# Kernel tuning notes

Hardware: AMD Instinct MI355X
Metric: run time of the kernel (lower is better)

## Reference

```python
import jax, jax.numpy as jnp
import numpy as np

BS, L, DIM = 16, 2048, 512
NUM_GROUPS, NUM_CODES = 2, 320
CODE_DIM = 256
VAR_DIM = CODE_DIM // NUM_GROUPS  # 128
INNER = DIM * 2                    # projFactor=2
TAU = 2.0                          # max(maxTemp*decay**0, minTemp) at numUpdates=0


def setup_inputs() -> dict:
    key = jax.random.key(0)
    ks = jax.random.split(key, 7)
    x = jax.random.normal(ks[0], (BS, L, DIM), jnp.float32)
    # gumbels = -log(Exp(1)) == standard Gumbel noise, matching torch's exponential_().log().neg()
    gumbels = jax.random.gumbel(ks[1], (BS * L * NUM_GROUPS, NUM_CODES), jnp.float32)
    W1 = jax.random.normal(ks[2], (DIM, INNER), jnp.float32) * (1.0 / np.sqrt(DIM))
    b1 = jnp.zeros((INNER,), jnp.float32)
    W2 = jax.random.normal(ks[3], (INNER, NUM_GROUPS * NUM_CODES), jnp.float32) * (1.0 / np.sqrt(INNER))
    b2 = jnp.zeros((NUM_GROUPS * NUM_CODES,), jnp.float32)
    # nn.init.uniform_ on embeddings: U[0,1); combineGroups=True -> single shared codebook (numCodes, varDim)
    emb = jax.random.uniform(ks[4], (NUM_CODES, VAR_DIM), jnp.float32)
    return {"x": x, "gumbels": gumbels, "W1": W1, "b1": b1, "W2": W2, "b2": b2, "emb": emb}


def reference(x, gumbels, W1, b1, W2, b2, emb):
    bs, l, d = x.shape
    xt = x.reshape(bs * l, d)
    h = jax.nn.gelu(xt @ W1 + b1, approximate=False)          # (N, INNER), torch GELU is exact erf
    logits = (h @ W2 + b2).reshape(bs * l * NUM_GROUPS, NUM_CODES)
    # training path: gumbel-softmax with straight-through hard one-hot
    soft = jax.nn.softmax((logits + gumbels) / TAU, axis=-1)  # (N*G, C)
    idx = jnp.argmax(soft, axis=-1)
    hard = jax.nn.one_hot(idx, NUM_CODES, dtype=soft.dtype)
    st = hard + soft - jax.lax.stop_gradient(soft)            # straight-through estimator
    st = st.reshape(bs * l, NUM_GROUPS, NUM_CODES)
    # combineGroups=True: embeddings repeated per group == shared codebook; the
    # (broadcast-mul).sum(-2) in torch is exactly this contraction (no huge intermediate).
    out = jnp.einsum('ngc,cd->ngd', st, emb)                  # (N, G, varDim)
    return out.reshape(bs, l, NUM_GROUPS * VAR_DIM)
```

## Files before the change

kernel.cpp:

```cpp
#include <hip/hip_runtime.h>
#include <math.h>


#define NTOK   32768
#define DIM    512
#define INNER  1024
#define NC     320
#define NGRP   2
#define VD     128
#define OUTD   256
#define RCAP   2048
#define W1F_OFF (1u<<20)
#define W2F_OFF (1u<<21)
#define HD_OFF  (1u<<22)
#define MARGIN 8.0e-3f
#define SMEM_BYTES (65536 + 3328)

typedef _Float16 half8 __attribute__((ext_vector_type(8)));
typedef _Float16 half4 __attribute__((ext_vector_type(4)));
typedef float    f32x4 __attribute__((ext_vector_type(4)));

#define W1F_N (16 * 64 * 64)
#define W2F_N (32 * 40 * 64)
__global__ void prep_kernel(const float* __restrict__ W1, const float* __restrict__ W2,
                            _Float16* __restrict__ W1F, _Float16* __restrict__ W2F,
                            unsigned* __restrict__ cnt) {
  const int o = blockIdx.x * 256 + threadIdx.x;
  if (o == 0) cnt[0] = 0u;
  if (o < W1F_N) {
    const int l = o & 63, ib = (o >> 6) & 63, ks = o >> 12;
    const int inner = ib * 16 + (l & 15);
    const int kb = ks * 32 + (l >> 4) * 8;
    _Float16* d = W1F + (size_t)o * 8;
#pragma unroll
    for (int j = 0; j < 8; ++j)
      d[j] = (_Float16)W1[(size_t)(kb + j) * INNER + inner];
  } else {
    const int o2 = o - W1F_N;
    if (o2 < W2F_N) {
      const int l = o2 & 63, cb = (o2 >> 6) % 40, ks = o2 / (40 * 64);
      const int code = cb * 16 + (l & 15);
      const int kb = ks * 32 + (l >> 4) * 8;
      _Float16* d = W2F + (size_t)o2 * 8;
#pragma unroll
      for (int j = 0; j < 8; ++j)
        d[j] = (_Float16)W2[(size_t)(kb + j) * (NC * NGRP) + code];
    }
  }
}

__device__ __forceinline__ float gelu_f(float s) {
  return 0.5f * s * (1.0f + erff(s * 0.70710678118654752440f));
}

__global__ __launch_bounds__(512, 4)
void fused_kernel(const float* __restrict__ x, const float* __restrict__ gum,
                  const _Float16* __restrict__ W1F, const _Float16* __restrict__ W2F,
                  const float* __restrict__ b1, const float* __restrict__ b2,
                  const float* __restrict__ emb, float* __restrict__ out,
                  unsigned* __restrict__ cnt, unsigned* __restrict__ list) {
  extern __shared__ char smem[];
  float*    redm1 = (float*)(smem + 65536);
  float*    redm2 = (float*)(smem + 65536 + 1024);
  unsigned* redi  = (unsigned*)(smem + 65536 + 2048);
  unsigned* idxs  = (unsigned*)(smem + 65536 + 3072);

  const int tid = threadIdx.x;
  const int w   = tid >> 6;
  const int l   = tid & 63;
  const int l15 = l & 15;
  const int lq  = l >> 4;
  const int T0  = blockIdx.x << 5;

#pragma unroll
  for (int i = 0; i < 8; ++i) {
    const int q = tid + i * 512;
    const int row = q >> 7;
    const int c = (q & 127) << 2;
    const float4 v = *(const float4*)(x + (size_t)(T0 + row) * DIM + c);
    half4 hv; hv[0] = (_Float16)v.x; hv[1] = (_Float16)v.y;
    hv[2] = (_Float16)v.z; hv[3] = (_Float16)v.w;
    const unsigned byte = ((unsigned)(row * 1024 + c * 2)) ^ ((unsigned)(row & 7) << 4);
    *(half4*)(smem + byte) = hv;
  }
  __syncthreads();

  {
    f32x4 acc[8][2];
#pragma unroll
    for (int i = 0; i < 8; ++i)
#pragma unroll
      for (int j = 0; j < 2; ++j) { f32x4 z = {0.f,0.f,0.f,0.f}; acc[i][j] = z; }

    const _Float16* w1f = W1F + (size_t)(w * 8) * 512 + (size_t)l * 8;
    for (int ks = 0; ks < 16; ++ks) {
      const int k0 = ks * 32;
      half8 a[8], bf[2];
#pragma unroll
      for (int mt = 0; mt < 8; ++mt)
        a[mt] = *(const half8*)(w1f + (size_t)(ks * 64 + mt) * 512);
#pragma unroll
      for (int nt = 0; nt < 2; ++nt) {
        const int token = nt * 16 + l15;
        const unsigned byte = ((unsigned)(token * 1024 + (k0 + lq * 8) * 2))
                              ^ ((unsigned)(token & 7) << 4);
        bf[nt] = *(const half8*)(smem + byte);
      }
#pragma unroll
      for (int mt = 0; mt < 8; ++mt)
#pragma unroll
        for (int nt = 0; nt < 2; ++nt)
          acc[mt][nt] = __builtin_amdgcn_mfma_f32_16x16x32_f16(a[mt], bf[nt], acc[mt][nt], 0, 0, 0);
    }
    __syncthreads();

#pragma unroll
    for (int mt = 0; mt < 8; ++mt) {
      const int inner0 = w * 128 + mt * 16 + lq * 4;
      const float4 bv = *(const float4*)(b1 + inner0);
#pragma unroll
      for (int nt = 0; nt < 2; ++nt) {
        const int token = nt * 16 + l15;
        const f32x4 v = acc[mt][nt];
        half4 hv;
        hv[0] = (_Float16)gelu_f(v[0] + bv.x);
        hv[1] = (_Float16)gelu_f(v[1] + bv.y);
        hv[2] = (_Float16)gelu_f(v[2] + bv.z);
        hv[3] = (_Float16)gelu_f(v[3] + bv.w);
        const unsigned byte = ((unsigned)(token * 2048 + inner0 * 2))
                              ^ ((unsigned)(token & 7) << 4);
        *(half4*)(smem + byte) = hv;
      }
    }
  }
  __syncthreads();

  const int g = w >> 2;
  {
    f32x4 acc[5][2];
#pragma unroll
    for (int i = 0; i < 5; ++i)
#pragma unroll
      for (int j = 0; j < 2; ++j) { f32x4 z = {0.f,0.f,0.f,0.f}; acc[i][j] = z; }

    const _Float16* w2f = W2F + (size_t)(w * 5) * 512 + (size_t)l * 8;
    for (int ks = 0; ks < 32; ++ks) {
      const int k0 = ks * 32;
      half8 a[5], bf[2];
#pragma unroll
      for (int mt = 0; mt < 5; ++mt)
        a[mt] = *(const half8*)(w2f + (size_t)(ks * 40 + mt) * 512);
#pragma unroll
      for (int nt = 0; nt < 2; ++nt) {
        const int token = nt * 16 + l15;
        const unsigned byte = ((unsigned)(token * 2048 + (k0 + lq * 8) * 2))
                              ^ ((unsigned)(token & 7) << 4);
        bf[nt] = *(const half8*)(smem + byte);
      }
#pragma unroll
      for (int mt = 0; mt < 5; ++mt)
#pragma unroll
        for (int nt = 0; nt < 2; ++nt)
          acc[mt][nt] = __builtin_amdgcn_mfma_f32_16x16x32_f16(a[mt], bf[nt], acc[mt][nt], 0, 0, 0);
    }

    float m1v[2] = {-1e30f,-1e30f};
    float m2v[2] = {-1e30f,-1e30f};
    unsigned i1v[2] = {0,0};
#pragma unroll
    for (int mt = 0; mt < 5; ++mt) {
      const int code0 = w * 80 + mt * 16 + lq * 4;
      const int cg0 = code0 - g * NC;
      const float4 b2v = *(const float4*)(b2 + code0);
#pragma unroll
      for (int nt = 0; nt < 2; ++nt) {
        const int tokg = T0 + nt * 16 + l15;
        const float4 gv = *(const float4*)(gum + ((size_t)tokg * 2 + g) * NC + cg0);
        const f32x4 v = acc[mt][nt];
        const float ss[4] = {v[0] + b2v.x + gv.x, v[1] + b2v.y + gv.y,
                             v[2] + b2v.z + gv.z, v[3] + b2v.w + gv.w};
#pragma unroll
        for (int r = 0; r < 4; ++r) {
          const float sv = ss[r];
          const unsigned cc = (unsigned)(cg0 + r);
          if (sv > m1v[nt]) { m2v[nt] = m1v[nt]; m1v[nt] = sv; i1v[nt] = cc; }
          else if (sv > m2v[nt]) m2v[nt] = sv;
        }
      }
    }
#pragma unroll
    for (int mask = 16; mask <= 32; mask <<= 1) {
#pragma unroll
      for (int nt = 0; nt < 2; ++nt) {
        const float om1 = __shfl_xor(m1v[nt], mask);
        const float om2 = __shfl_xor(m2v[nt], mask);
        const unsigned oi = (unsigned)__shfl_xor((int)i1v[nt], mask);
        const bool take = (om1 > m1v[nt]) || (om1 == m1v[nt] && oi < i1v[nt]);
        if (take) { m2v[nt] = fmaxf(m1v[nt], om2); m1v[nt] = om1; i1v[nt] = oi; }
        else      { m2v[nt] = fmaxf(m2v[nt], om1); }
      }
    }
    if (l < 16) {
#pragma unroll
      for (int nt = 0; nt < 2; ++nt) {
        const int tok = nt * 16 + l15;
        redm1[w * 32 + tok] = m1v[nt];
        redm2[w * 32 + tok] = m2v[nt];
        redi [w * 32 + tok] = i1v[nt];
      }
    }
  }
  __syncthreads();

  if (tid < 64) {
    const int pg = tid >> 5;
    const int tok = tid & 31;
    float m1 = -1e30f, m2 = -1e30f; unsigned i1 = 0;
#pragma unroll
    for (int k = 0; k < 4; ++k) {
      const int ww = pg * 4 + k;
      const float a1 = redm1[ww * 32 + tok];
      const float a2 = redm2[ww * 32 + tok];
      const unsigned ai = redi[ww * 32 + tok];
      if (a1 > m1) { m2 = fmaxf(m1, a2); m1 = a1; i1 = ai; }
      else         { m2 = fmaxf(m2, a1); }
    }
    idxs[tid] = i1;
    if (m1 - m2 < MARGIN) {
      const unsigned pos = atomicAdd(cnt, 1u);
      if (pos < RCAP) list[pos] = (unsigned)(((T0 + tok) << 1) | pg);
    }
  }
  __syncthreads();

#pragma unroll
  for (int i = 0; i < 4; ++i) {
    const int q = tid + i * 512;
    const int p = q >> 5;
    const int dd = q & 31;
    const int pg = p >> 5;
    const int tok = p & 31;
    const unsigned idx = idxs[p];
    *(float4*)(out + (size_t)(T0 + tok) * OUTD + pg * VD + dd * 4)
      = *(const float4*)(emb + (size_t)idx * VD + dd * 4);
  }
}

__global__ __launch_bounds__(512, 4)
void refine1_kernel(const float* __restrict__ x, const float* __restrict__ W1,
                    const float* __restrict__ b1,
                    const unsigned* __restrict__ cnt, const unsigned* __restrict__ list,
                    float* __restrict__ hdws) {
  __shared__ float xs[DIM];
  unsigned n = cnt[0]; if (n > RCAP) n = RCAP;
  const unsigned e = blockIdx.x;
  if (e >= n) return;
  const unsigned tok = list[e] >> 1;
  const int tid = threadIdx.x;
  xs[tid] = x[(size_t)tok * DIM + tid];
  __syncthreads();

  double a0 = 0.0, a1 = 0.0, c0 = 0.0, c1 = 0.0;
#pragma unroll 4
  for (int k = 0; k < DIM; k += 2) {
    const double x0 = (double)xs[k], x1 = (double)xs[k + 1];
    const float* r0 = W1 + (size_t)k * INNER + tid;
    const float* r1 = W1 + (size_t)(k + 1) * INNER + tid;
    a0 += x0 * (double)r0[0];
    a1 += x0 * (double)r0[512];
    c0 += x1 * (double)r1[0];
    c1 += x1 * (double)r1[512];
  }
  const double s0 = a0 + c0 + (double)b1[tid];
  const double s1 = a1 + c1 + (double)b1[tid + 512];
  hdws[(size_t)e * INNER + tid]       = (float)(0.5 * s0 * (1.0 + erf(s0 * 0.70710678118654752440)));
  hdws[(size_t)e * INNER + tid + 512] = (float)(0.5 * s1 * (1.0 + erf(s1 * 0.70710678118654752440)));
}

__global__ __launch_bounds__(320, 4)
void refine2_kernel(const float* __restrict__ gum, const float* __restrict__ W2,
                    const float* __restrict__ b2, const float* __restrict__ emb,
                    float* __restrict__ out,
                    const unsigned* __restrict__ cnt, const unsigned* __restrict__ list,
                    const float* __restrict__ hdws) {
  __shared__ float hs[INNER];
  __shared__ double wv[5];
  __shared__ int wi[5];
  __shared__ int best;
  unsigned n = cnt[0]; if (n > RCAP) n = RCAP;
  const unsigned e = blockIdx.x;
  if (e >= n) return;
  const unsigned tok = list[e] >> 1;
  const int g = (int)(list[e] & 1u);
  const int tid = threadIdx.x;

  for (int j = tid; j < INNER; j += 320) hs[j] = hdws[(size_t)e * INNER + j];
  __syncthreads();

  const float* w2c = W2 + (size_t)g * NC + tid;
  double acc = 0.0, accb = 0.0;
#pragma unroll 4
  for (int k = 0; k < INNER; k += 2) {
    acc  += (double)hs[k]     * (double)w2c[(size_t)k * (NC * NGRP)];
    accb += (double)hs[k + 1] * (double)w2c[(size_t)(k + 1) * (NC * NGRP)];
  }
  double v = acc + accb + (double)b2[g * NC + tid]
                        + (double)gum[((size_t)tok * 2 + g) * NC + tid];
  int bi = tid;
#pragma unroll
  for (int m = 1; m < 64; m <<= 1) {
    const double ov = __shfl_xor(v, m);
    const int oi = __shfl_xor(bi, m);
    if (ov > v || (ov == v && oi < bi)) { v = ov; bi = oi; }
  }
  if ((tid & 63) == 0) { wv[tid >> 6] = v; wi[tid >> 6] = bi; }
  __syncthreads();
  if (tid == 0) {
    double bv = wv[0]; int bb = wi[0];
#pragma unroll
    for (int k = 1; k < 5; ++k)
      if (wv[k] > bv || (wv[k] == bv && wi[k] < bb)) { bv = wv[k]; bb = wi[k]; }
    best = bb;
  }
  __syncthreads();
  if (tid < VD)
    out[(size_t)tok * OUTD + g * VD + tid] = emb[(size_t)best * VD + tid];
}

__global__ __launch_bounds__(512, 1)
void refine_kernel(const float* __restrict__ x, const float* __restrict__ gum,
                   const float* __restrict__ W1, const float* __restrict__ b1,
                   const float* __restrict__ W2, const float* __restrict__ b2,
                   const float* __restrict__ emb, float* __restrict__ out,
                   const unsigned* __restrict__ cnt, const unsigned* __restrict__ list) {
  __shared__ double xs[4][DIM];
  __shared__ double hd[4][INNER];
  __shared__ double sc[4][NC];
  __shared__ int amax[4];
  const int tid = threadIdx.x;
  unsigned n = cnt[0];
  if (n > RCAP) n = RCAP;

  for (unsigned base = blockIdx.x * 4u; base < n; base += gridDim.x * 4u) {
    const int nb = (int)((n - base) < 4u ? (n - base) : 4u);
    unsigned ng[4];
#pragma unroll
    for (int e = 0; e < 4; ++e) ng[e] = list[base + (e < nb ? e : 0)];

    for (int e = 0; e < nb; ++e)
      xs[e][tid] = (double)x[(size_t)(ng[e] >> 1) * DIM + tid];
    __syncthreads();

#pragma unroll
    for (int jj = 0; jj < 2; ++jj) {
      const int j = tid + jj * 512;
      double a0 = 0, a1 = 0, a2 = 0, a3 = 0;
      for (int k = 0; k < DIM; ++k) {
        const double wvv = (double)W1[(size_t)k * INNER + j];
        a0 += xs[0][k] * wvv; a1 += xs[1][k] * wvv;
        a2 += xs[2][k] * wvv; a3 += xs[3][k] * wvv;
      }
      const double bb = (double)b1[j];
      const double s0 = a0 + bb, s1 = a1 + bb, s2 = a2 + bb, s3 = a3 + bb;
      hd[0][j] = 0.5 * s0 * (1.0 + erf(s0 * 0.70710678118654752440));
      hd[1][j] = 0.5 * s1 * (1.0 + erf(s1 * 0.70710678118654752440));
      hd[2][j] = 0.5 * s2 * (1.0 + erf(s2 * 0.70710678118654752440));
      hd[3][j] = 0.5 * s3 * (1.0 + erf(s3 * 0.70710678118654752440));
    }
    __syncthreads();

    for (int task = tid; task < 4 * NC; task += 512) {
      const int e = task / NC;
      const int c = task - e * NC;
      if (e < nb) {
        const unsigned tok = ng[e] >> 1;
        const int gg = (int)(ng[e] & 1u);
        const float* w2c = W2 + (size_t)gg * NC + c;
        double acc = 0.0;
        for (int k = 0; k < INNER; ++k)
          acc += hd[e][k] * (double)w2c[(size_t)k * (NC * NGRP)];
        sc[e][c] = acc + (double)b2[gg * NC + c]
                       + (double)gum[((size_t)tok * 2 + gg) * NC + c];
      }
    }
    __syncthreads();

    if (tid < 4 && tid < nb) {
      double bestv = sc[tid][0]; int bi = 0;
      for (int c = 1; c < NC; ++c)
        if (sc[tid][c] > bestv) { bestv = sc[tid][c]; bi = c; }
      amax[tid] = bi;
    }
    __syncthreads();

    {
      const int e = tid >> 7;
      const int d = tid & 127;
      if (e < nb) {
        const unsigned tok = ng[e] >> 1;
        const int gg = (int)(ng[e] & 1u);
        out[(size_t)tok * OUTD + gg * VD + d] = emb[(size_t)amax[e] * VD + d];
      }
    }
    __syncthreads();
  }
}

extern "C" void kernel_launch(void* const* d_in, const int* in_sizes, int n_in,
                              void* d_out, int out_size, void* d_ws, size_t ws_size,
                              hipStream_t stream) {
  (void)in_sizes; (void)n_in; (void)out_size;
  const float* x   = (const float*)d_in[0];
  const float* gum = (const float*)d_in[1];
  const float* W1  = (const float*)d_in[2];
  const float* b1  = (const float*)d_in[3];
  const float* W2  = (const float*)d_in[4];
  const float* b2  = (const float*)d_in[5];
  const float* emb = (const float*)d_in[6];
  float* out = (float*)d_out;
  char* ws = (char*)d_ws;
  unsigned* cnt  = (unsigned*)ws;
  unsigned* list = (unsigned*)(ws + 16);
  _Float16* W1F = (_Float16*)(ws + W1F_OFF);
  _Float16* W2F = (_Float16*)(ws + W2F_OFF);
  float* hdws = (float*)(ws + HD_OFF);

  hipFuncSetAttribute((const void*)fused_kernel,
                      hipFuncAttributeMaxDynamicSharedMemorySize, SMEM_BYTES);

  const int prep_items = W1F_N + W2F_N;
  prep_kernel<<<(prep_items + 255) / 256, 256, 0, stream>>>(W1, W2, W1F, W2F, cnt);
  fused_kernel<<<NTOK / 32, 512, SMEM_BYTES, stream>>>(x, gum, W1F, W2F, b1, b2,
                                                       emb, out, cnt, list);
  const bool big_ws = ws_size >= (size_t)HD_OFF + (size_t)RCAP * INNER * sizeof(float);
  if (big_ws) {
    refine1_kernel<<<RCAP, 512, 0, stream>>>(x, W1, b1, cnt, list, hdws);
    refine2_kernel<<<RCAP, 320, 0, stream>>>(gum, W2, b2, emb, out, cnt, list, hdws);
  } else {
    refine_kernel<<<256, 512, 0, stream>>>(x, gum, W1, b1, W2, b2, emb, out, cnt, list);
  }
}
```

Before: 269.2 us.

## Split fused MLP into tiled fp16 GEMM kernels with LDS-direct loads

Replaces the per-32-token fused kernel with separate kernels: a prep pass converting x and weights to fp16, a 128x128-tiled GEMM1 with GELU writing h to workspace, a tiled GEMM2 computing per-tile top-2 partials, and a reduce kernel that picks the argmax and gathers embeddings. Loads go through global_load_lds into swizzled shared memory. The aim is more weight reuse per block and better MFMA utilisation. The cost is extra global round trips for xh, h and the partials, plus more kernel launches. The old fused path is kept as a fallback for small workspaces.

```diff
diff --git a/kernel.cpp b/kernel.cpp
--- a/kernel.cpp
+++ b/kernel.cpp
@@ -10,239 +10,294 @@
 #define VD     128
 #define OUTD   256
 #define RCAP   2048
+#define MARGIN 8.0e-3f
+
+#define L_LIST 16u
+#define L_W1T  (64u<<10)
+#define L_W2T  (2u<<20)
+#define L_XH   (4u<<20)
+#define L_H    (36u<<20)
+#define L_PART (100u<<20)
+#define L_HDW  (104u<<20)
+#define WS_NEED (120u<<20)
+
 #define W1F_OFF (1u<<20)
 #define W2F_OFF (1u<<21)
-#define HD_OFF  (1u<<22)
-#define MARGIN 8.0e-3f
 #define SMEM_BYTES (65536 + 3328)
 
 typedef _Float16 half8 __attribute__((ext_vector_type(8)));
 typedef _Float16 half4 __attribute__((ext_vector_type(4)));
 typedef float    f32x4 __attribute__((ext_vector_type(4)));
 
-#define W1F_N (16 * 64 * 64)
-#define W2F_N (32 * 40 * 64)
-__global__ void prep_kernel(const float* __restrict__ W1, const float* __restrict__ W2,
-                            _Float16* __restrict__ W1F, _Float16* __restrict__ W2F,
-                            unsigned* __restrict__ cnt) {
+__device__ __forceinline__ float gelu_f(float s) {
+  return 0.5f * s * (1.0f + erff(s * 0.70710678118654752440f));
+}
+
+#if defined(__has_builtin) && __has_builtin(__builtin_amdgcn_global_load_lds)
+#define GLOAD16(gp, ldsbase, lane) \
+  __builtin_amdgcn_global_load_lds((const __attribute__((address_space(1))) void*)(gp), \
+                                   (__attribute__((address_space(3))) void*)(ldsbase), 16, 0, 0)
+#else
+#define GLOAD16(gp, ldsbase, lane) \
+  do { *(uint4*)((char*)(ldsbase) + (lane) * 16) = *(const uint4*)(gp); } while (0)
+#endif
+
+#define XH_JOBS   2097152
+#define W1T_JOBS  65536
+#define W2T_JOBS  81920
+#define PREP_JOBS (XH_JOBS + W1T_JOBS + W2T_JOBS)
+__global__ __launch_bounds__(256)
+void prep2_kernel(const float* __restrict__ x, const float* __restrict__ W1,
+                  const float* __restrict__ W2, _Float16* __restrict__ xh,
+                  _Float16* __restrict__ W1T, _Float16* __restrict__ W2T,
+                  unsigned* __restrict__ cnt) {
   const int o = blockIdx.x * 256 + threadIdx.x;
   if (o == 0) cnt[0] = 0u;
-  if (o < W1F_N) {
-    const int l = o & 63, ib = (o >> 6) & 63, ks = o >> 12;
-    const int inner = ib * 16 + (l & 15);
-    const int kb = ks * 32 + (l >> 4) * 8;
-    _Float16* d = W1F + (size_t)o * 8;
+  if (o < XH_JOBS) {
+    const float4 v0 = *(const float4*)(x + (size_t)o * 8);
+    const float4 v1 = *(const float4*)(x + (size_t)o * 8 + 4);
+    half8 hv;
+    hv[0] = (_Float16)v0.x; hv[1] = (_Float16)v0.y; hv[2] = (_Float16)v0.z; hv[3] = (_Float16)v0.w;
+    hv[4] = (_Float16)v1.x; hv[5] = (_Float16)v1.y; hv[6] = (_Float16)v1.z; hv[7] = (_Float16)v1.w;
+    *(half8*)(xh + (size_t)o * 8) = hv;
+  } else if (o < XH_JOBS + W1T_JOBS) {
+    const int q = o - XH_JOBS;
+    const int i = q >> 6, k0 = (q & 63) * 8;
 #pragma unroll
     for (int j = 0; j < 8; ++j)
-      d[j] = (_Float16)W1[(size_t)(kb + j) * INNER + inner];
-  } else {
-    const int o2 = o - W1F_N;
-    if (o2 < W2F_N) {
-      const int l = o2 & 63, cb = (o2 >> 6) % 40, ks = o2 / (40 * 64);
-      const int code = cb * 16 + (l & 15);
-      const int kb = ks * 32 + (l >> 4) * 8;
-      _Float16* d = W2F + (size_t)o2 * 8;
-#pragma unroll
-      for (int j = 0; j < 8; ++j)
-        d[j] = (_Float16)W2[(size_t)(kb + j) * (NC * NGRP) + code];
-    }
-  }
-}
-
-__device__ __forceinline__ float gelu_f(float s) {
-  return 0.5f * s * (1.0f + erff(s * 0.70710678118654752440f));
-}
-
-__global__ __launch_bounds__(512, 4)
-void fused_kernel(const float* __restrict__ x, const float* __restrict__ gum,
-                  const _Float16* __restrict__ W1F, const _Float16* __restrict__ W2F,
-                  const float* __restrict__ b1, const float* __restrict__ b2,
-                  const float* __restrict__ emb, float* __restrict__ out,
-                  unsigned* __restrict__ cnt, unsigned* __restrict__ list) {
-  extern __shared__ char smem[];
-  float*    redm1 = (float*)(smem + 65536);
-  float*    redm2 = (float*)(smem + 65536 + 1024);
-  unsigned* redi  = (unsigned*)(smem + 65536 + 2048);
-  unsigned* idxs  = (unsigned*)(smem + 65536 + 3072);
-
+      W1T[(size_t)i * DIM + k0 + j] = (_Float16)W1[(size_t)(k0 + j) * INNER + i];
+  } else if (o < PREP_JOBS) {
+    const int q = o - XH_JOBS - W1T_JOBS;
+    const int c = q >> 7, i0 = (q & 127) * 8;
+#pragma unroll
+    for (int j = 0; j < 8; ++j)
+      W2T[(size_t)c * INNER + i0 + j] = (_Float16)W2[(size_t)(i0 + j) * (NC * NGRP) + c];
+  }
+}
+
+__global__ __launch_bounds__(256, 4)
+void gemm1_kernel(const _Float16* __restrict__ xh, const _Float16* __restrict__ W1T,
+                  const float* __restrict__ b1, _Float16* __restrict__ h) {
+  __shared__ char smem[32768];
   const int tid = threadIdx.x;
-  const int w   = tid >> 6;
-  const int l   = tid & 63;
-  const int l15 = l & 15;
-  const int lq  = l >> 4;
-  const int T0  = blockIdx.x << 5;
-
-#pragma unroll
-  for (int i = 0; i < 8; ++i) {
-    const int q = tid + i * 512;
-    const int row = q >> 7;
-    const int c = (q & 127) << 2;
-    const float4 v = *(const float4*)(x + (size_t)(T0 + row) * DIM + c);
-    half4 hv; hv[0] = (_Float16)v.x; hv[1] = (_Float16)v.y;
-    hv[2] = (_Float16)v.z; hv[3] = (_Float16)v.w;
-    const unsigned byte = ((unsigned)(row * 1024 + c * 2)) ^ ((unsigned)(row & 7) << 4);
-    *(half4*)(smem + byte) = hv;
-  }
-  __syncthreads();
-
-  {
-    f32x4 acc[8][2];
-#pragma unroll
-    for (int i = 0; i < 8; ++i)
-#pragma unroll
-      for (int j = 0; j < 2; ++j) { f32x4 z = {0.f,0.f,0.f,0.f}; acc[i][j] = z; }
-
-    const _Float16* w1f = W1F + (size_t)(w * 8) * 512 + (size_t)l * 8;
-    for (int ks = 0; ks < 16; ++ks) {
-      const int k0 = ks * 32;
-      half8 a[8], bf[2];
-#pragma unroll
-      for (int mt = 0; mt < 8; ++mt)
-        a[mt] = *(const half8*)(w1f + (size_t)(ks * 64 + mt) * 512);
-#pragma unroll
-      for (int nt = 0; nt < 2; ++nt) {
-        const int token = nt * 16 + l15;
-        const unsigned byte = ((unsigned)(token * 1024 + (k0 + lq * 8) * 2))
-                              ^ ((unsigned)(token & 7) << 4);
-        bf[nt] = *(const half8*)(smem + byte);
-      }
-#pragma unroll
-      for (int mt = 0; mt < 8; ++mt)
-#pragma unroll
-        for (int nt = 0; nt < 2; ++nt)
-          acc[mt][nt] = __builtin_amdgcn_mfma_f32_16x16x32_f16(a[mt], bf[nt], acc[mt][nt], 0, 0, 0);
-    }
-    __syncthreads();
-
-#pragma unroll
-    for (int mt = 0; mt < 8; ++mt) {
-      const int inner0 = w * 128 + mt * 16 + lq * 4;
-      const float4 bv = *(const float4*)(b1 + inner0);
-#pragma unroll
-      for (int nt = 0; nt < 2; ++nt) {
-        const int token = nt * 16 + l15;
-        const f32x4 v = acc[mt][nt];
-        half4 hv;
-        hv[0] = (_Float16)gelu_f(v[0] + bv.x);
-        hv[1] = (_Float16)gelu_f(v[1] + bv.y);
-        hv[2] = (_Float16)gelu_f(v[2] + bv.z);
-        hv[3] = (_Float16)gelu_f(v[3] + bv.w);
-        const unsigned byte = ((unsigned)(token * 2048 + inner0 * 2))
-                              ^ ((unsigned)(token & 7) << 4);
-        *(half4*)(smem + byte) = hv;
-      }
-    }
-  }
-  __syncthreads();
-
-  const int g = w >> 2;
-  {
-    f32x4 acc[5][2];
-#pragma unroll
-    for (int i = 0; i < 5; ++i)
-#pragma unroll
-      for (int j = 0; j < 2; ++j) { f32x4 z = {0.f,0.f,0.f,0.f}; acc[i][j] = z; }
-
-    const _Float16* w2f = W2F + (size_t)(w * 5) * 512 + (size_t)l * 8;
-    for (int ks = 0; ks < 32; ++ks) {
-      const int k0 = ks * 32;
-      half8 a[5], bf[2];
-#pragma unroll
-      for (int mt = 0; mt < 5; ++mt)
-        a[mt] = *(const half8*)(w2f + (size_t)(ks * 40 + mt) * 512);
-#pragma unroll
-      for (int nt = 0; nt < 2; ++nt) {
-        const int token = nt * 16 + l15;
-        const unsigned byte = ((unsigned)(token * 2048 + (k0 + lq * 8) * 2))
-                              ^ ((unsigned)(token & 7) << 4);
-        bf[nt] = *(const half8*)(smem + byte);
-      }
-#pragma unroll
-      for (int mt = 0; mt < 5; ++mt)
-#pragma unroll
-        for (int nt = 0; nt < 2; ++nt)
-          acc[mt][nt] = __builtin_amdgcn_mfma_f32_16x16x32_f16(a[mt], bf[nt], acc[mt][nt], 0, 0, 0);
-    }
-
-    float m1v[2] = {-1e30f,-1e30f};
-    float m2v[2] = {-1e30f,-1e30f};
-    unsigned i1v[2] = {0,0};
-#pragma unroll
-    for (int mt = 0; mt < 5; ++mt) {
-      const int code0 = w * 80 + mt * 16 + lq * 4;
-      const int cg0 = code0 - g * NC;
-      const float4 b2v = *(const float4*)(b2 + code0);
-#pragma unroll
-      for (int nt = 0; nt < 2; ++nt) {
-        const int tokg = T0 + nt * 16 + l15;
-        const float4 gv = *(const float4*)(gum + ((size_t)tokg * 2 + g) * NC + cg0);
-        const f32x4 v = acc[mt][nt];
-        const float ss[4] = {v[0] + b2v.x + gv.x, v[1] + b2v.y + gv.y,
-                             v[2] + b2v.z + gv.z, v[3] + b2v.w + gv.w};
-#pragma unroll
-        for (int r = 0; r < 4; ++r) {
-          const float sv = ss[r];
-          const unsigned cc = (unsigned)(cg0 + r);
-          if (sv > m1v[nt]) { m2v[nt] = m1v[nt]; m1v[nt] = sv; i1v[nt] = cc; }
-          else if (sv > m2v[nt]) m2v[nt] = sv;
+  const int w = tid >> 6, l = tid & 63;
+  const int l15 = l & 15, lq = l >> 4;
+  const int bid = blockIdx.x;
+  const int bn = bid & 7, bm = bid >> 3;
+  const int wm = w >> 1, wn = w & 1;
+
+  const int r0 = (w * 2 + 0) * 16 + (l >> 2);
+  const int r1 = (w * 2 + 1) * 16 + (l >> 2);
+  const int c0 = (((l & 3) ^ (r0 & 3)) * 8);
+  const int c1 = (((l & 3) ^ (r1 & 3)) * 8);
+  const _Float16* gA0 = xh  + (size_t)(bm * 128 + r0) * DIM + c0;
+  const _Float16* gA1 = xh  + (size_t)(bm * 128 + r1) * DIM + c1;
+  const _Float16* gB0 = W1T + (size_t)(bn * 128 + r0) * DIM + c0;
+  const _Float16* gB1 = W1T + (size_t)(bn * 128 + r1) * DIM + c1;
+  char* lA0 = smem + (w * 2 + 0) * 1024;
+  char* lA1 = smem + (w * 2 + 1) * 1024;
+  char* lB0 = smem + 8192 + (w * 2 + 0) * 1024;
+  char* lB1 = smem + 8192 + (w * 2 + 1) * 1024;
+
+  f32x4 acc[4][4];
+#pragma unroll
+  for (int i = 0; i < 4; ++i)
+#pragma unroll
+    for (int j = 0; j < 4; ++j) { f32x4 z = {0.f, 0.f, 0.f, 0.f}; acc[i][j] = z; }
+
+  const int swz = (lq ^ (l15 & 3)) << 4;
+  const int aoff = (wm * 64 + l15) * 64 + swz;
+  const int boff = 8192 + (wn * 64 + l15) * 64 + swz;
+
+  for (int ks = 0; ks < 16; ++ks) {
+    __syncthreads();
+    GLOAD16(gA0 + ks * 32, lA0, l);
+    GLOAD16(gA1 + ks * 32, lA1, l);
+    GLOAD16(gB0 + ks * 32, lB0, l);
+    GLOAD16(gB1 + ks * 32, lB1, l);
+    __syncthreads();
+    half8 a[4], b[4];
+#pragma unroll
+    for (int mi = 0; mi < 4; ++mi) a[mi] = *(const half8*)(smem + aoff + mi * 1024);
+#pragma unroll
+    for (int ni = 0; ni < 4; ++ni) b[ni] = *(const half8*)(smem + boff + ni * 1024);
+#pragma unroll
+    for (int mi = 0; mi < 4; ++mi)
+#pragma unroll
+      for (int ni = 0; ni < 4; ++ni)
+        acc[mi][ni] = __builtin_amdgcn_mfma_f32_16x16x32_f16(a[mi], b[ni], acc[mi][ni], 0, 0, 0);
+  }
+  __syncthreads();
+
+  _Float16* eT = (_Float16*)smem;
+  float bb[4];
+#pragma unroll
+  for (int ni = 0; ni < 4; ++ni) bb[ni] = b1[bn * 128 + wn * 64 + ni * 16 + l15];
+#pragma unroll
+  for (int mi = 0; mi < 4; ++mi) {
+    const int row = wm * 64 + mi * 16 + lq * 4;
+#pragma unroll
+    for (int ni = 0; ni < 4; ++ni) {
+      const int col = wn * 64 + ni * 16 + l15;
+#pragma unroll
+      for (int r = 0; r < 4; ++r)
+        eT[(row + r) * 128 + col] = (_Float16)gelu_f(acc[mi][ni][r] + bb[ni]);
+    }
+  }
+  __syncthreads();
+#pragma unroll
+  for (int it = 0; it < 8; ++it) {
+    const int s = tid + it * 256;
+    const int row = s >> 4, i8 = s & 15;
+    *(half8*)(h + (size_t)(bm * 128 + row) * INNER + bn * 128 + i8 * 8)
+        = *(const half8*)(eT + row * 128 + i8 * 8);
+  }
+}
+
+__global__ __launch_bounds__(256, 4)
+void gemm2_kernel(const _Float16* __restrict__ h, const _Float16* __restrict__ W2T,
+                  const float* __restrict__ b2, const float* __restrict__ gum,
+                  unsigned* __restrict__ part) {
+  __shared__ char smem[32768];
+  const int tid = threadIdx.x;
+  const int w = tid >> 6, l = tid & 63;
+  const int l15 = l & 15, lq = l >> 4;
+  const int bid = blockIdx.x;
+  const int bt = bid % 5, bm = bid / 5;
+  const int wm = w >> 1, wn = w & 1;
+
+  const int r0 = (w * 2 + 0) * 16 + (l >> 2);
+  const int r1 = (w * 2 + 1) * 16 + (l >> 2);
+  const int c0 = (((l & 3) ^ (r0 & 3)) * 8);
+  const int c1 = (((l & 3) ^ (r1 & 3)) * 8);
+  const _Float16* gA0 = h   + (size_t)(bm * 128 + r0) * INNER + c0;
+  const _Float16* gA1 = h   + (size_t)(bm * 128 + r1) * INNER + c1;
+  const _Float16* gB0 = W2T + (size_t)(bt * 128 + r0) * INNER + c0;
+  const _Float16* gB1 = W2T + (size_t)(bt * 128 + r1) * INNER + c1;
+  char* lA0 = smem + (w * 2 + 0) * 1024;
+  char* lA1 = smem + (w * 2 + 1) * 1024;
+  char* lB0 = smem + 8192 + (w * 2 + 0) * 1024;
+  char* lB1 = smem + 8192 + (w * 2 + 1) * 1024;
+
+  f32x4 acc[4][4];
+#pragma unroll
+  for (int i = 0; i < 4; ++i)
+#pragma unroll
+    for (int j = 0; j < 4; ++j) { f32x4 z = {0.f, 0.f, 0.f, 0.f}; acc[i][j] = z; }
+
+  const int swz = (lq ^ (l15 & 3)) << 4;
+  const int aoff = (wm * 64 + l15) * 64 + swz;
+  const int boff = 8192 + (wn * 64 + l15) * 64 + swz;
+
+  for (int ks = 0; ks < 32; ++ks) {
+    __syncthreads();
+    GLOAD16(gA0 + ks * 32, lA0, l);
+    GLOAD16(gA1 + ks * 32, lA1, l);
+    GLOAD16(gB0 + ks * 32, lB0, l);
+    GLOAD16(gB1 + ks * 32, lB1, l);
+    __syncthreads();
+    half8 a[4], b[4];
+#pragma unroll
+    for (int mi = 0; mi < 4; ++mi) a[mi] = *(const half8*)(smem + aoff + mi * 1024);
+#pragma unroll
+    for (int ni = 0; ni < 4; ++ni) b[ni] = *(const half8*)(smem + boff + ni * 1024);
+#pragma unroll
+    for (int mi = 0; mi < 4; ++mi)
+#pragma unroll
+      for (int ni = 0; ni < 4; ++ni)
+        acc[mi][ni] = __builtin_amdgcn_mfma_f32_16x16x32_f16(a[mi], b[ni], acc[mi][ni], 0, 0, 0);
+  }
+
+  float* eF = (float*)smem;
+  const int nm = (bt == 2) ? 8 : 16;
+#pragma unroll
+  for (int half = 0; half < 2; ++half) {
+    __syncthreads();
+    if (wm == half) {
+#pragma unroll
+      for (int mi = 0; mi < 4; ++mi) {
+        const int rl = mi * 16 + lq * 4;
+#pragma unroll
+        for (int ni = 0; ni < 4; ++ni) {
+          const int col = wn * 64 + ni * 16 + l15;
+#pragma unroll
+          for (int r = 0; r < 4; ++r) eF[(rl + r) * 128 + col] = acc[mi][ni][r];
         }
       }
     }
-#pragma unroll
-    for (int mask = 16; mask <= 32; mask <<= 1) {
-#pragma unroll
-      for (int nt = 0; nt < 2; ++nt) {
-        const float om1 = __shfl_xor(m1v[nt], mask);
-        const float om2 = __shfl_xor(m2v[nt], mask);
-        const unsigned oi = (unsigned)__shfl_xor((int)i1v[nt], mask);
-        const bool take = (om1 > m1v[nt]) || (om1 == m1v[nt] && oi < i1v[nt]);
-        if (take) { m2v[nt] = fmaxf(m1v[nt], om2); m1v[nt] = om1; i1v[nt] = oi; }
-        else      { m2v[nt] = fmaxf(m2v[nt], om1); }
-      }
-    }
-    if (l < 16) {
-#pragma unroll
-      for (int nt = 0; nt < 2; ++nt) {
-        const int tok = nt * 16 + l15;
-        redm1[w * 32 + tok] = m1v[nt];
-        redm2[w * 32 + tok] = m2v[nt];
-        redi [w * 32 + tok] = i1v[nt];
-      }
-    }
-  }
-  __syncthreads();
-
-  if (tid < 64) {
-    const int pg = tid >> 5;
-    const int tok = tid & 31;
-    float m1 = -1e30f, m2 = -1e30f; unsigned i1 = 0;
-#pragma unroll
-    for (int k = 0; k < 4; ++k) {
-      const int ww = pg * 4 + k;
-      const float a1 = redm1[ww * 32 + tok];
-      const float a2 = redm2[ww * 32 + tok];
-      const unsigned ai = redi[ww * 32 + tok];
-      if (a1 > m1) { m2 = fmaxf(m1, a2); m1 = a1; i1 = ai; }
-      else         { m2 = fmaxf(m2, a1); }
-    }
-    idxs[tid] = i1;
-    if (m1 - m2 < MARGIN) {
-      const unsigned pos = atomicAdd(cnt, 1u);
-      if (pos < RCAP) list[pos] = (unsigned)(((T0 + tok) << 1) | pg);
-    }
-  }
-  __syncthreads();
-
-#pragma unroll
-  for (int i = 0; i < 4; ++i) {
-    const int q = tid + i * 512;
-    const int p = q >> 5;
-    const int dd = q & 31;
-    const int pg = p >> 5;
-    const int tok = p & 31;
-    const unsigned idx = idxs[p];
-    *(float4*)(out + (size_t)(T0 + tok) * OUTD + pg * VD + dd * 4)
-      = *(const float4*)(emb + (size_t)idx * VD + dd * 4);
+    __syncthreads();
+#pragma unroll
+    for (int it = 0; it < 8; ++it) {
+      const int s = tid + it * 256;
+      const int rl = s >> 5, cc = (s & 31) * 4;
+      const int t = bm * 128 + half * 64 + rl;
+      const float4 lv  = *(const float4*)(eF + rl * 128 + cc);
+      const float4 b2v = *(const float4*)(b2 + bt * 128 + cc);
+      const float4 gv  = *(const float4*)(gum + (size_t)t * 640 + bt * 128 + cc);
+      float m1 = -1e30f, m2 = -1e30f; unsigned i1 = 0;
+      const float vv[4] = {(lv.x + b2v.x) + gv.x, (lv.y + b2v.y) + gv.y,
+                           (lv.z + b2v.z) + gv.z, (lv.w + b2v.w) + gv.w};
+#pragma unroll
+      for (int r = 0; r < 4; ++r) {
+        const unsigned c = (unsigned)(bt * 128 + cc + r);
+        if (vv[r] > m1) { m2 = m1; m1 = vv[r]; i1 = c; }
+        else if (vv[r] > m2) m2 = vv[r];
+      }
+      for (int m = 1; m <= nm; m <<= 1) {
+        const float om1 = __shfl_xor(m1, m);
+        const float om2 = __shfl_xor(m2, m);
+        const unsigned oi = (unsigned)__shfl_xor((int)i1, m);
+        const bool take = (om1 > m1) || (om1 == m1 && oi < i1);
+        if (take) { m2 = fmaxf(m1, om2); m1 = om1; i1 = oi; }
+        else      { m2 = fmaxf(m2, om1); }
+      }
+      const int lr = tid & 31;
+      const bool writer = (bt == 2) ? (lr == 0 || lr == 16) : (lr == 0);
+      if (writer) {
+        int slot;
+        if (bt == 0) slot = 0; else if (bt == 1) slot = 1;
+        else if (bt == 3) slot = 4; else if (bt == 4) slot = 5;
+        else slot = (i1 < (unsigned)NC) ? 2 : 3;
+        const unsigned ing = (i1 < (unsigned)NC) ? i1 : (i1 - NC);
+        unsigned* p = part + ((size_t)t * 6 + slot) * 4;
+        p[0] = __float_as_uint(m1);
+        p[1] = __float_as_uint(m2);
+        p[2] = ing;
+      }
+    }
+  }
+}
+
+__global__ __launch_bounds__(256, 4)
+void reduce_kernel(const unsigned* __restrict__ part, const float* __restrict__ emb,
+                   float* __restrict__ out, unsigned* __restrict__ cnt,
+                   unsigned* __restrict__ list) {
+  __shared__ unsigned idxs[256];
+  const int tid = threadIdx.x;
+  const int pair = blockIdx.x * 256 + tid;
+  const int t = pair >> 1, g = pair & 1;
+  float m1 = -1e30f, m2 = -1e30f; unsigned i1 = 0;
+#pragma unroll
+  for (int s = 0; s < 3; ++s) {
+    const unsigned* p = part + ((size_t)t * 6 + g * 3 + s) * 4;
+    const float a1 = __uint_as_float(p[0]);
+    const float a2 = __uint_as_float(p[1]);
+    const unsigned ai = p[2];
+    if (a1 > m1) { m2 = fmaxf(m1, a2); m1 = a1; i1 = ai; }
+    else         { m2 = fmaxf(m2, a1); }
+  }
+  idxs[tid] = i1;
+  if (m1 - m2 < MARGIN) {
+    const unsigned pos = atomicAdd(cnt, 1u);
+    if (pos < RCAP) list[pos] = (unsigned)((t << 1) | g);
+  }
+  __syncthreads();
+#pragma unroll
+  for (int it = 0; it < 32; ++it) {
+    const int s2 = tid + it * 256;
+    const int p = s2 >> 5, dd = (s2 & 31) * 4;
+    *(float4*)(out + (size_t)blockIdx.x * 32768 + p * 128 + dd)
+        = *(const float4*)(emb + (size_t)idxs[p] * VD + dd);
   }
 }
 
@@ -259,17 +314,16 @@
   const int tid = threadIdx.x;
   xs[tid] = x[(size_t)tok * DIM + tid];
   __syncthreads();
-
   double a0 = 0.0, a1 = 0.0, c0 = 0.0, c1 = 0.0;
 #pragma unroll 4
   for (int k = 0; k < DIM; k += 2) {
     const double x0 = (double)xs[k], x1 = (double)xs[k + 1];
-    const float* r0 = W1 + (size_t)k * INNER + tid;
-    const float* r1 = W1 + (size_t)(k + 1) * INNER + tid;
-    a0 += x0 * (double)r0[0];
-    a1 += x0 * (double)r0[512];
-    c0 += x1 * (double)r1[0];
-    c1 += x1 * (double)r1[512];
+    const float* rr0 = W1 + (size_t)k * INNER + tid;
+    const float* rr1 = W1 + (size_t)(k + 1) * INNER + tid;
+    a0 += x0 * (double)rr0[0];
+    a1 += x0 * (double)rr0[512];
+    c0 += x1 * (double)rr1[0];
+    c1 += x1 * (double)rr1[512];
   }
   const double s0 = a0 + c0 + (double)b1[tid];
   const double s1 = a1 + c1 + (double)b1[tid + 512];
@@ -293,10 +347,8 @@
   const unsigned tok = list[e] >> 1;
   const int g = (int)(list[e] & 1u);
   const int tid = threadIdx.x;
-
   for (int j = tid; j < INNER; j += 320) hs[j] = hdws[(size_t)e * INNER + j];
   __syncthreads();
-
   const float* w2c = W2 + (size_t)g * NC + tid;
   double acc = 0.0, accb = 0.0;
 #pragma unroll 4
@@ -325,6 +377,212 @@
   __syncthreads();
   if (tid < VD)
     out[(size_t)tok * OUTD + g * VD + tid] = emb[(size_t)best * VD + tid];
+}
+
+#define W1F_N (16 * 64 * 64)
+#define W2F_N (32 * 40 * 64)
+__global__ void prep_kernel(const float* __restrict__ W1, const float* __restrict__ W2,
+                            _Float16* __restrict__ W1F, _Float16* __restrict__ W2F,
+                            unsigned* __restrict__ cnt) {
+  const int o = blockIdx.x * 256 + threadIdx.x;
+  if (o == 0) cnt[0] = 0u;
+  if (o < W1F_N) {
+    const int l = o & 63, ib = (o >> 6) & 63, ks = o >> 12;
+    const int inner = ib * 16 + (l & 15);
+    const int kb = ks * 32 + (l >> 4) * 8;
+    _Float16* d = W1F + (size_t)o * 8;
+#pragma unroll
+    for (int j = 0; j < 8; ++j) d[j] = (_Float16)W1[(size_t)(kb + j) * INNER + inner];
+  } else {
+    const int o2 = o - W1F_N;
+    if (o2 < W2F_N) {
+      const int l = o2 & 63, cb = (o2 >> 6) % 40, ks = o2 / (40 * 64);
+      const int code = cb * 16 + (l & 15);
+      const int kb = ks * 32 + (l >> 4) * 8;
+      _Float16* d = W2F + (size_t)o2 * 8;
+#pragma unroll
+      for (int j = 0; j < 8; ++j) d[j] = (_Float16)W2[(size_t)(kb + j) * (NC * NGRP) + code];
+    }
+  }
+}
+
+__global__ __launch_bounds__(512, 4)
+void fused_kernel(const float* __restrict__ x, const float* __restrict__ gum,
+                  const _Float16* __restrict__ W1F, const _Float16* __restrict__ W2F,
+                  const float* __restrict__ b1, const float* __restrict__ b2,
+                  const float* __restrict__ emb, float* __restrict__ out,
+                  unsigned* __restrict__ cnt, unsigned* __restrict__ list) {
+  extern __shared__ char smem[];
+  float*    redm1 = (float*)(smem + 65536);
+  float*    redm2 = (float*)(smem + 65536 + 1024);
+  unsigned* redi  = (unsigned*)(smem + 65536 + 2048);
+  unsigned* idxs  = (unsigned*)(smem + 65536 + 3072);
+  const int tid = threadIdx.x;
+  const int w = tid >> 6, l = tid & 63;
+  const int l15 = l & 15, lq = l >> 4;
+  const int T0 = blockIdx.x << 5;
+#pragma unroll
+  for (int i = 0; i < 8; ++i) {
+    const int q = tid + i * 512;
+    const int row = q >> 7;
+    const int c = (q & 127) << 2;
+    const float4 v = *(const float4*)(x + (size_t)(T0 + row) * DIM + c);
+    half4 hv; hv[0] = (_Float16)v.x; hv[1] = (_Float16)v.y;
+    hv[2] = (_Float16)v.z; hv[3] = (_Float16)v.w;
+    const unsigned byte = ((unsigned)(row * 1024 + c * 2)) ^ ((unsigned)(row & 7) << 4);
+    *(half4*)(smem + byte) = hv;
+  }
+  __syncthreads();
+  {
+    f32x4 acc[8][2];
+#pragma unroll
+    for (int i = 0; i < 8; ++i)
+#pragma unroll
+      for (int j = 0; j < 2; ++j) { f32x4 z = {0.f,0.f,0.f,0.f}; acc[i][j] = z; }
+    const _Float16* w1f = W1F + (size_t)(w * 8) * 512 + (size_t)l * 8;
+    for (int ks = 0; ks < 16; ++ks) {
+      const int k0 = ks * 32;
+      half8 a[8], bf[2];
+#pragma unroll
+      for (int mt = 0; mt < 8; ++mt) a[mt] = *(const half8*)(w1f + (size_t)(ks * 64 + mt) * 512);
+#pragma unroll
+      for (int nt = 0; nt < 2; ++nt) {
+        const int token = nt * 16 + l15;
+        const unsigned byte = ((unsigned)(token * 1024 + (k0 + lq * 8) * 2))
+                              ^ ((unsigned)(token & 7) << 4);
+        bf[nt] = *(const half8*)(smem + byte);
+      }
+#pragma unroll
+      for (int mt = 0; mt < 8; ++mt)
+#pragma unroll
+        for (int nt = 0; nt < 2; ++nt)
+          acc[mt][nt] = __builtin_amdgcn_mfma_f32_16x16x32_f16(a[mt], bf[nt], acc[mt][nt], 0, 0, 0);
+    }
+    __syncthreads();
+#pragma unroll
+    for (int mt = 0; mt < 8; ++mt) {
+      const int inner0 = w * 128 + mt * 16 + lq * 4;
+      const float4 bv = *(const float4*)(b1 + inner0);
+#pragma unroll
+      for (int nt = 0; nt < 2; ++nt) {
+        const int token = nt * 16 + l15;
+        const f32x4 v = acc[mt][nt];
+        half4 hv;
+        hv[0] = (_Float16)gelu_f(v[0] + bv.x);
+        hv[1] = (_Float16)gelu_f(v[1] + bv.y);
+        hv[2] = (_Float16)gelu_f(v[2] + bv.z);
+        hv[3] = (_Float16)gelu_f(v[3] + bv.w);
+        const unsigned byte = ((unsigned)(token * 2048 + inner0 * 2))
+                              ^ ((unsigned)(token & 7) << 4);
+        *(half4*)(smem + byte) = hv;
+      }
+    }
+  }
+  __syncthreads();
+  const int g = w >> 2;
+  {
+    f32x4 acc[5][2];
+#pragma unroll
+    for (int i = 0; i < 5; ++i)
+#pragma unroll
+      for (int j = 0; j < 2; ++j) { f32x4 z = {0.f,0.f,0.f,0.f}; acc[i][j] = z; }
+    const _Float16* w2f = W2F + (size_t)(w * 5) * 512 + (size_t)l * 8;
+    for (int ks = 0; ks < 32; ++ks) {
+      const int k0 = ks * 32;
+      half8 a[5], bf[2];
+#pragma unroll
+      for (int mt = 0; mt < 5; ++mt) a[mt] = *(const half8*)(w2f + (size_t)(ks * 40 + mt) * 512);
+#pragma unroll
+      for (int nt = 0; nt < 2; ++nt) {
+        const int token = nt * 16 + l15;
+        const unsigned byte = ((unsigned)(token * 2048 + (k0 + lq * 8) * 2))
+                              ^ ((unsigned)(token & 7) << 4);
+        bf[nt] = *(const half8*)(smem + byte);
+      }
+#pragma unroll
+      for (int mt = 0; mt < 5; ++mt)
+#pragma unroll
+        for (int nt = 0; nt < 2; ++nt)
+          acc[mt][nt] = __builtin_amdgcn_mfma_f32_16x16x32_f16(a[mt], bf[nt], acc[mt][nt], 0, 0, 0);
+    }
+    float m1v[2] = {-1e30f,-1e30f};
+    float m2v[2] = {-1e30f,-1e30f};
+    unsigned i1v[2] = {0,0};
+#pragma unroll
+    for (int mt = 0; mt < 5; ++mt) {
+      const int code0 = w * 80 + mt * 16 + lq * 4;
+      const int cg0 = code0 - g * NC;
+      const float4 b2v = *(const float4*)(b2 + code0);
+#pragma unroll
+      for (int nt = 0; nt < 2; ++nt) {
+        const int tokg = T0 + nt * 16 + l15;
+        const float4 gv = *(const float4*)(gum + ((size_t)tokg * 2 + g) * NC + cg0);
+        const f32x4 v = acc[mt][nt];
+        const float ss[4] = {v[0] + b2v.x + gv.x, v[1] + b2v.y + gv.y,
+                             v[2] + b2v.z + gv.z, v[3] + b2v.w + gv.w};
+#pragma unroll
+        for (int r = 0; r < 4; ++r) {
+          const float sv = ss[r];
+          const unsigned cc = (unsigned)(cg0 + r);
+          if (sv > m1v[nt]) { m2v[nt] = m1v[nt]; m1v[nt] = sv; i1v[nt] = cc; }
+          else if (sv > m2v[nt]) m2v[nt] = sv;
+        }
+      }
+    }
+#pragma unroll
+    for (int mask = 16; mask <= 32; mask <<= 1) {
+#pragma unroll
+      for (int nt = 0; nt < 2; ++nt) {
+        const float om1 = __shfl_xor(m1v[nt], mask);
+        const float om2 = __shfl_xor(m2v[nt], mask);
+        const unsigned oi = (unsigned)__shfl_xor((int)i1v[nt], mask);
+        const bool take = (om1 > m1v[nt]) || (om1 == m1v[nt] && oi < i1v[nt]);
+        if (take) { m2v[nt] = fmaxf(m1v[nt], om2); m1v[nt] = om1; i1v[nt] = oi; }
+        else      { m2v[nt] = fmaxf(m2v[nt], om1); }
+      }
+    }
+    if (l < 16) {
+#pragma unroll
+      for (int nt = 0; nt < 2; ++nt) {
+        const int tok = nt * 16 + l15;
+        redm1[w * 32 + tok] = m1v[nt];
+        redm2[w * 32 + tok] = m2v[nt];
+        redi [w * 32 + tok] = i1v[nt];
+      }
+    }
+  }
+  __syncthreads();
+  if (tid < 64) {
+    const int pg = tid >> 5;
+    const int tok = tid & 31;
+    float m1 = -1e30f, m2 = -1e30f; unsigned i1 = 0;
+#pragma unroll
+    for (int k = 0; k < 4; ++k) {
+      const int ww = pg * 4 + k;
+      const float a1 = redm1[ww * 32 + tok];
+      const float a2 = redm2[ww * 32 + tok];
+      const unsigned ai = redi[ww * 32 + tok];
+      if (a1 > m1) { m2 = fmaxf(m1, a2); m1 = a1; i1 = ai; }
+      else         { m2 = fmaxf(m2, a1); }
+    }
+    idxs[tid] = i1;
+    if (m1 - m2 < MARGIN) {
+      const unsigned pos = atomicAdd(cnt, 1u);
+      if (pos < RCAP) list[pos] = (unsigned)(((T0 + tok) << 1) | pg);
+    }
+  }
+  __syncthreads();
+#pragma unroll
+  for (int i = 0; i < 4; ++i) {
+    const int q = tid + i * 512;
+    const int p = q >> 5;
+    const int dd = q & 31;
+    const int pg = p >> 5;
+    const int tok = p & 31;
+    const unsigned idx = idxs[p];
+    *(float4*)(out + (size_t)(T0 + tok) * OUTD + pg * VD + dd * 4)
+      = *(const float4*)(emb + (size_t)idx * VD + dd * 4);
+  }
 }
 
 __global__ __launch_bounds__(512, 1)
@@ -340,17 +598,14 @@
   const int tid = threadIdx.x;
   unsigned n = cnt[0];
   if (n > RCAP) n = RCAP;
-
   for (unsigned base = blockIdx.x * 4u; base < n; base += gridDim.x * 4u) {
     const int nb = (int)((n - base) < 4u ? (n - base) : 4u);
     unsigned ng[4];
 #pragma unroll
     for (int e = 0; e < 4; ++e) ng[e] = list[base + (e < nb ? e : 0)];
-
     for (int e = 0; e < nb; ++e)
       xs[e][tid] = (double)x[(size_t)(ng[e] >> 1) * DIM + tid];
     __syncthreads();
-
 #pragma unroll
     for (int jj = 0; jj < 2; ++jj) {
       const int j = tid + jj * 512;
@@ -368,7 +623,6 @@
       hd[3][j] = 0.5 * s3 * (1.0 + erf(s3 * 0.70710678118654752440));
     }
     __syncthreads();
-
     for (int task = tid; task < 4 * NC; task += 512) {
       const int e = task / NC;
       const int c = task - e * NC;
@@ -384,7 +638,6 @@
       }
     }
     __syncthreads();
-
     if (tid < 4 && tid < nb) {
       double bestv = sc[tid][0]; int bi = 0;
       for (int c = 1; c < NC; ++c)
@@ -392,7 +645,6 @@
       amax[tid] = bi;
     }
     __syncthreads();
-
     {
       const int e = tid >> 7;
       const int d = tid & 127;
@@ -420,23 +672,31 @@
   float* out = (float*)d_out;
   char* ws = (char*)d_ws;
   unsigned* cnt  = (unsigned*)ws;
-  unsigned* list = (unsigned*)(ws + 16);
-  _Float16* W1F = (_Float16*)(ws + W1F_OFF);
-  _Float16* W2F = (_Float16*)(ws + W2F_OFF);
-  float* hdws = (float*)(ws + HD_OFF);
-
-  hipFuncSetAttribute((const void*)fused_kernel,
-                      hipFuncAttributeMaxDynamicSharedMemorySize, SMEM_BYTES);
-
-  const int prep_items = W1F_N + W2F_N;
-  prep_kernel<<<(prep_items + 255) / 256, 256, 0, stream>>>(W1, W2, W1F, W2F, cnt);
-  fused_kernel<<<NTOK / 32, 512, SMEM_BYTES, stream>>>(x, gum, W1F, W2F, b1, b2,
-                                                       emb, out, cnt, list);
-  const bool big_ws = ws_size >= (size_t)HD_OFF + (size_t)RCAP * INNER * sizeof(float);
-  if (big_ws) {
+  unsigned* list = (unsigned*)(ws + L_LIST);
+
+  if (ws_size >= (size_t)WS_NEED) {
+    _Float16* W1T = (_Float16*)(ws + L_W1T);
+    _Float16* W2T = (_Float16*)(ws + L_W2T);
+    _Float16* xh  = (_Float16*)(ws + L_XH);
+    _Float16* h   = (_Float16*)(ws + L_H);
+    unsigned* part = (unsigned*)(ws + L_PART);
+    float* hdws = (float*)(ws + L_HDW);
+
+    prep2_kernel<<<(PREP_JOBS + 255) / 256, 256, 0, stream>>>(x, W1, W2, xh, W1T, W2T, cnt);
+    gemm1_kernel<<<(NTOK / 128) * 8, 256, 0, stream>>>(xh, W1T, b1, h);
+    gemm2_kernel<<<(NTOK / 128) * 5, 256, 0, stream>>>(h, W2T, b2, gum, part);
+    reduce_kernel<<<NTOK * NGRP / 256, 256, 0, stream>>>(part, emb, out, cnt, list);
     refine1_kernel<<<RCAP, 512, 0, stream>>>(x, W1, b1, cnt, list, hdws);
     refine2_kernel<<<RCAP, 320, 0, stream>>>(gum, W2, b2, emb, out, cnt, list, hdws);
   } else {
+    _Float16* W1F = (_Float16*)(ws + W1F_OFF);
+    _Float16* W2F = (_Float16*)(ws + W2F_OFF);
+    hipFuncSetAttribute((const void*)fused_kernel,
+                        hipFuncAttributeMaxDynamicSharedMemorySize, SMEM_BYTES);
+    const int prep_items = W1F_N + W2F_N;
+    prep_kernel<<<(prep_items + 255) / 256, 256, 0, stream>>>(W1, W2, W1F, W2F, cnt);
+    fused_kernel<<<NTOK / 32, 512, SMEM_BYTES, stream>>>(x, gum, W1F, W2F, b1, b2,
+                                                         emb, out, cnt, list);
     refine_kernel<<<256, 512, 0, stream>>>(x, gum, W1, b1, W2, b2, emb, out, cnt, list);
   }
 }
```

Result: slower. 334.5 us (+24.3%).
